# Kernel tuning notes

Measured on AMD Instinct MI355X. Metric: run time of the kernel, lower is better.

## Reference

```python
import jax, jax.numpy as jnp
import numpy as np

BETA = 0.25
EMA_DECAY = 0.99
EMA_EPS = 1e-05
K = 8192
D = 512


def setup_inputs() -> dict:
    key = jax.random.key(0)
    k1, k2, k3, k4 = jax.random.split(key, 4)
    z = jax.random.normal(k1, (8, 2048, D), dtype=jnp.float32)
    codebook_weight = jax.random.normal(k2, (K, D), dtype=jnp.float32)
    ema_cluster_size = jax.random.uniform(k3, (K,), dtype=jnp.float32)
    ema_embed_avg = jax.random.normal(k4, (K, D), dtype=jnp.float32)
    return {"z": z, "codebook_weight": codebook_weight,
            "ema_cluster_size": ema_cluster_size, "ema_embed_avg": ema_embed_avg}


def reference(z, codebook_weight, ema_cluster_size, ema_embed_avg):
    d = z.shape[-1]
    flat = z.reshape(-1, d)                                  # [N, D]
    z_sq = jnp.sum(flat * flat, axis=1, keepdims=True)       # [N, 1]
    e = codebook_weight                                      # [K, D]
    e_sq = jnp.sum(e * e, axis=1)                            # [K]
    # logits = -||z - e||^2 (argmax over logits == nearest code)
    logits = -(z_sq - 2.0 * jnp.matmul(flat, e.T) + e_sq)    # [N, K]
    idx = jnp.argmax(logits, axis=1)                         # [N]
    z_q = e[idx].reshape(z.shape)

    # commitment loss: beta * sum((z - sg[z_q])^2) / D
    vq_loss = BETA * jnp.sum((z - jax.lax.stop_gradient(z_q)) ** 2) / d

    # EMA statistics (torch.no_grad block)
    flat_sg = jax.lax.stop_gradient(flat)
    n_codes = e.shape[0]
    ones = jnp.ones(flat.shape[0], dtype=flat.dtype)
    cluster_size = jax.ops.segment_sum(ones, idx, num_segments=n_codes)       # == onehot.sum(0)
    embed_sum = jax.ops.segment_sum(flat_sg, idx, num_segments=n_codes)       # == onehot.T @ flat
    new_ema_cluster_size = ema_cluster_size * EMA_DECAY + cluster_size * (1.0 - EMA_DECAY)
    new_ema_embed_avg = ema_embed_avg * EMA_DECAY + embed_sum * (1.0 - EMA_DECAY)
    updated = new_ema_embed_avg / (new_ema_cluster_size[:, None] + EMA_EPS)
    active = (cluster_size > 0)[:, None]
    new_codebook = jnp.where(active, updated, codebook_weight)
    # (random reseeding of never-used codes is intentionally omitted: it is
    # nondeterministic and outside the deterministic math path)

    # straight-through estimator
    z_out = z + jax.lax.stop_gradient(z_q - z)
    return (z_out, vq_loss, new_ema_cluster_size, new_ema_embed_avg, new_codebook)
```

## Files before the change

### kernel.cpp

```cpp
#include <hip/hip_runtime.h>
#include <hip/hip_bf16.h>

#define N_ROWS 16384
#define DDIM   512
#define KCODES 8192
#define BETA   0.25f
#define DECAY  0.99f
#define ONE_MINUS_DECAY 0.01f
#define EMA_EPS 1e-5f

#define O_Z    0
#define O_LOSS 8388608
#define O_CS   8388609
#define O_AVG  8396801
#define O_CB   12591105

#define WS_CNT      0
#define WS_ESQ      32768
#define WS_FLAGCNT  65536
#define WS_FLAGLIST 65792
#define WS_KEYS     73984
#define WS_SEC2     205056
#define WS_LOSSP    270592
#define WS_IDXS     270848
#define WS_OFFS     336384
#define WS_CURS     369152
#define WS_ROWLIST  401920
#define WS_Z16      467456
#define WS_CB16     17244672

#define TAU  0.35f
#define RCAP 2048

typedef _Float16 half8  __attribute__((ext_vector_type(8)));
typedef float    floatx4 __attribute__((ext_vector_type(4)));

__device__ __forceinline__ unsigned enc_f(float d) {
    unsigned ub = __float_as_uint(d);
    return (ub & 0x80000000u) ? ~ub : (ub | 0x80000000u);
}
__device__ __forceinline__ float dec32(unsigned ub) {
    return __uint_as_float((ub & 0x80000000u) ? (ub ^ 0x80000000u) : ~ub);
}
__device__ __forceinline__ float dec_key(unsigned long long k) {
    return dec32((unsigned)(k >> 32));
}

__device__ __forceinline__ float4 pack8_f16(float4 a, float4 b) {
    auto p0 = __builtin_amdgcn_cvt_pkrtz(a.x, a.y);
    auto p1 = __builtin_amdgcn_cvt_pkrtz(a.z, a.w);
    auto p2 = __builtin_amdgcn_cvt_pkrtz(b.x, b.y);
    auto p3 = __builtin_amdgcn_cvt_pkrtz(b.z, b.w);
    float4 r;
    r.x = __builtin_bit_cast(float, p0);
    r.y = __builtin_bit_cast(float, p1);
    r.z = __builtin_bit_cast(float, p2);
    r.w = __builtin_bit_cast(float, p3);
    return r;
}

__device__ __forceinline__ void load_lds16(const void* g, void* l) {
    __builtin_amdgcn_global_load_lds(
        (const __attribute__((address_space(1))) unsigned int*)g,
        (__attribute__((address_space(3))) unsigned int*)l, 16, 0, 0);
}

__global__ __launch_bounds__(256) void cvtz_kernel(const float* __restrict__ z,
                                                   _Float16* __restrict__ z16,
                                                   unsigned long long* __restrict__ keys,
                                                   unsigned* __restrict__ sec2,
                                                   float* __restrict__ lossp,
                                                   int* __restrict__ flagcnt) {
    size_t i = (size_t)blockIdx.x * 256 + threadIdx.x;
    const float4* p = (const float4*)z + 2 * i;
    ((float4*)z16)[i] = pack8_f16(p[0], p[1]);
    if (i < N_ROWS) { keys[i] = ~0ULL; sec2[i] = 0xFFFFFFFFu; }
    if (i < 64) lossp[i] = 0.0f;
    if (i == 0) *flagcnt = 0;
}

__global__ __launch_bounds__(64) void cvtcb_kernel(const float* __restrict__ cb,
                                                   _Float16* __restrict__ cb16,
                                                   float* __restrict__ e_sq,
                                                   int* __restrict__ cnt) {
    int k = blockIdx.x;
    int t = threadIdx.x;
    const float4* r = (const float4*)(cb + (size_t)k * DDIM);
    float4 a = r[2 * t], b = r[2 * t + 1];
    ((float4*)(cb16 + (size_t)k * DDIM))[t] = pack8_f16(a, b);
    float s = a.x*a.x + a.y*a.y + a.z*a.z + a.w*a.w
            + b.x*b.x + b.y*b.y + b.z*b.z + b.w*b.w;
    #pragma unroll
    for (int o = 32; o > 0; o >>= 1) s += __shfl_down(s, o);
    if (t == 0) { e_sq[k] = s; cnt[k] = 0; }
}

__global__ __launch_bounds__(256, 4) void screen_kernel(
    const _Float16* __restrict__ z16, const _Float16* __restrict__ cb16,
    const float* __restrict__ e_sq,
    unsigned long long* __restrict__ keys, unsigned* __restrict__ sec2) {
    __shared__ _Float16 zt[128 * 64];
    __shared__ _Float16 ct[128 * 64];

    const int tid = threadIdx.x;
    const int by = blockIdx.x;
    const int bx = blockIdx.y;
    const int lane = tid & 63, wid = tid >> 6;
    const int wm = wid & 1, wn = wid >> 1;
    const int lr = lane & 15, lq = lane >> 4;

    const _Float16* zsrc[4]; const _Float16* csrc[4];
    #pragma unroll
    for (int r = 0; r < 4; r++) {
        int g = (r * 4 + wid) * 64 + lane;
        int row = g >> 3, kq = g & 7;
        zsrc[r] = z16 + (size_t)(by * 128 + row) * DDIM + ((kq ^ (row & 7)) << 3);
        csrc[r] = cb16 + (size_t)(bx * 128 + row) * DDIM + ((kq ^ (row & 7)) << 3);
    }

    floatx4 acc[4][4];
    #pragma unroll
    for (int i = 0; i < 4; i++)
        #pragma unroll
        for (int j = 0; j < 4; j++) acc[i][j] = floatx4{0.f, 0.f, 0.f, 0.f};

    for (int kc = 0; kc < DDIM; kc += 64) {
        #pragma unroll
        for (int r = 0; r < 4; r++) load_lds16(zsrc[r] + kc, &zt[(r * 4 + wid) * 512]);
        #pragma unroll
        for (int r = 0; r < 4; r++) load_lds16(csrc[r] + kc, &ct[(r * 4 + wid) * 512]);
        __syncthreads();
        #pragma unroll
        for (int kk = 0; kk < 2; kk++) {
            half8 av[4];
            #pragma unroll
            for (int mt = 0; mt < 4; mt++) {
                int row = wm * 64 + mt * 16 + lr;
                av[mt] = *(const half8*)&zt[row * 64 + (((kk * 4 + lq) ^ (row & 7)) << 3)];
            }
            #pragma unroll
            for (int nt = 0; nt < 4; nt++) {
                int row = wn * 64 + nt * 16 + lr;
                half8 bv = *(const half8*)&ct[row * 64 + (((kk * 4 + lq) ^ (row & 7)) << 3)];
                #pragma unroll
                for (int mt = 0; mt < 4; mt++)
                    acc[mt][nt] = __builtin_amdgcn_mfma_f32_16x16x32_f16(av[mt], bv, acc[mt][nt], 0, 0, 0);
            }
        }
        __syncthreads();
    }

    float* eb_d1 = (float*)zt;
    int*   eb_c1 = (int*)zt + 256;
    float* eb_d2 = (float*)zt + 512;

    float es[4];
    #pragma unroll
    for (int nt = 0; nt < 4; nt++) es[nt] = e_sq[bx * 128 + wn * 64 + nt * 16 + lr];

    #pragma unroll
    for (int mt = 0; mt < 4; mt++) {
        #pragma unroll
        for (int r = 0; r < 4; r++) {
            float d1 = 1e30f, d2 = 1e30f; int c1 = 0x7FFFFFFF;
            #pragma unroll
            for (int nt = 0; nt < 4; nt++) {
                float d = fmaf(-2.0f, acc[mt][nt][r], es[nt]);
                int c = bx * 128 + wn * 64 + nt * 16 + lr;
                bool better = (d < d1) || (d == d1 && c < c1);
                if (better) { d2 = d1; d1 = d; c1 = c; }
                else        { d2 = fminf(d2, d); }
            }
            #pragma unroll
            for (int off = 1; off < 16; off <<= 1) {
                float od1 = __shfl_xor(d1, off);
                int   oc1 = __shfl_xor(c1, off);
                float od2 = __shfl_xor(d2, off);
                bool better = (od1 < d1) || (od1 == d1 && oc1 < c1);
                if (better) { d2 = fminf(d1, od2); d1 = od1; c1 = oc1; }
                else        { d2 = fminf(d2, od1); }
            }
            if (lr == 0) {
                int row = wm * 64 + mt * 16 + lq * 4 + r;
                eb_d1[wn * 128 + row] = d1; eb_c1[wn * 128 + row] = c1; eb_d2[wn * 128 + row] = d2;
            }
        }
    }
    __syncthreads();
    if (tid < 128) {
        float d1a = eb_d1[tid],       d2a = eb_d2[tid];       int c1a = eb_c1[tid];
        float d1b = eb_d1[128 + tid], d2b = eb_d2[128 + tid]; int c1b = eb_c1[128 + tid];
        bool bbet = (d1b < d1a) || (d1b == d1a && c1b < c1a);
        float d1 = bbet ? d1b : d1a; int c1 = bbet ? c1b : c1a;
        float d2 = bbet ? fminf(d1a, d2b) : fminf(d2a, d1b);
        unsigned long long key = ((unsigned long long)enc_f(d1) << 32) | (unsigned)c1;
        int row_g = by * 128 + tid;
        unsigned long long old = atomicMin(&keys[row_g], key);
        float cand = (key < old) ? fminf(dec_key(old), d2) : fminf(d1, d2);
        atomicMin(&sec2[row_g], enc_f(cand));
    }
}

__global__ void merge_kernel(unsigned long long* __restrict__ keys,
                             const unsigned* __restrict__ sec2,
                             int* __restrict__ flagcnt, int* __restrict__ flaglist) {
    int row = blockIdx.x * 256 + threadIdx.x;
    unsigned long long kb = keys[row];
    float best = dec_key(kb);
    float sec  = dec32(sec2[row]);
    if (sec - best < TAU) {
        int pos = atomicAdd(flagcnt, 1);
        if (pos < RCAP) { flaglist[pos] = row; keys[row] = ~0ULL; }
    }
}

__global__ __launch_bounds__(256) void rescore_kernel(
    const float* __restrict__ z, const float* __restrict__ cb,
    const float* __restrict__ e_sq, const int* __restrict__ flagcnt,
    const int* __restrict__ flaglist, unsigned long long* __restrict__ keys) {
    int n = *flagcnt; n = min(n, RCAP);
    int base = blockIdx.y * 64;
    if (base >= n) return;
    __shared__ float ech[64][132];
    __shared__ float zch[64][68];
    __shared__ int ridx[64];
    const int tid = threadIdx.x;
    const int bx = blockIdx.x;
    if (tid < 64) ridx[tid] = flaglist[min(base + tid, n - 1)];
    __syncthreads();

    const int tc = tid & 15;
    const int tg = tid >> 4;

    float es[8];
    #pragma unroll
    for (int c = 0; c < 8; c++) es[c] = e_sq[bx * 128 + tc * 8 + c];

    float acc[4][8] = {};
    for (int kc = 0; kc < DDIM; kc += 64) {
        #pragma unroll
        for (int l = 0; l < 8; l++) {
            int gi = tid + 256 * l;
            int code = gi >> 4, q = gi & 15;
            float4 v = *(const float4*)&cb[(size_t)(bx * 128 + code) * DDIM + kc + q * 4];
            ech[q * 4 + 0][code] = v.x; ech[q * 4 + 1][code] = v.y;
            ech[q * 4 + 2][code] = v.z; ech[q * 4 + 3][code] = v.w;
        }
        #pragma unroll
        for (int l = 0; l < 4; l++) {
            int gi = tid + 256 * l;
            int row = gi >> 4, q = gi & 15;
            float4 v = *(const float4*)&z[(size_t)ridx[row] * DDIM + kc + q * 4];
            zch[q * 4 + 0][row] = v.x; zch[q * 4 + 1][row] = v.y;
            zch[q * 4 + 2][row] = v.z; zch[q * 4 + 3][row] = v.w;
        }
        __syncthreads();
        for (int k = 0; k < 64; k++) {
            const float4 b0 = *(const float4*)&ech[k][tc * 8];
            const float4 b1 = *(const float4*)&ech[k][tc * 8 + 4];
            const float4 a  = *(const float4*)&zch[k][tg * 4];
            const float ar[4] = {a.x, a.y, a.z, a.w};
            const float br[8] = {b0.x, b0.y, b0.z, b0.w, b1.x, b1.y, b1.z, b1.w};
            #pragma unroll
            for (int r = 0; r < 4; r++)
                #pragma unroll
                for (int c = 0; c < 8; c++)
                    acc[r][c] = fmaf(ar[r], br[c], acc[r][c]);
        }
        __syncthreads();
    }

    unsigned long long (*redk)[17] = (unsigned long long (*)[17])&ech[0][0];
    #pragma unroll
    for (int r = 0; r < 4; r++) {
        unsigned long long bk = ~0ULL;
        #pragma unroll
        for (int c = 0; c < 8; c++) {
            int code = bx * 128 + tc * 8 + c;
            float d = fmaf(-2.0f, acc[r][c], es[c]);
            unsigned long long key = ((unsigned long long)enc_f(d) << 32) | (unsigned)code;
            bk = (key < bk) ? key : bk;
        }
        redk[tg * 4 + r][tc] = bk;
    }
    __syncthreads();
    if (tid < 64) {
        unsigned long long b = redk[tid][0];
        #pragma unroll
        for (int t = 1; t < 16; t++) {
            unsigned long long v = redk[tid][t];
            b = (v < b) ? v : b;
        }
        atomicMin(&keys[ridx[tid]], b);
    }
}

__global__ __launch_bounds__(256) void zout_loss_kernel(
    const float* __restrict__ z, const float* __restrict__ cb,
    const unsigned long long* __restrict__ keys,
    float* __restrict__ out, int* __restrict__ cnt,
    int* __restrict__ idxs, float* __restrict__ lossp) {
    const int tid = threadIdx.x;
    const int sub = tid >> 7;
    const int t   = tid & 127;
    const int row = blockIdx.x * 2 + sub;
    const int idx = (int)(unsigned int)(keys[row] & 0xFFFFFFFFull);

    const float4 zv = ((const float4*)(z  + (size_t)row * DDIM))[t];
    const float4 ev = ((const float4*)(cb + (size_t)idx * DDIM))[t];
    ((float4*)(out + O_Z + (size_t)row * DDIM))[t] = ev;

    float dx = zv.x - ev.x, dy = zv.y - ev.y, dz = zv.z - ev.z, dw = zv.w - ev.w;
    float s = dx*dx + dy*dy + dz*dz + dw*dw;

    #pragma unroll
    for (int o = 32; o > 0; o >>= 1) s += __shfl_down(s, o);
    __shared__ float red[4];
    if ((tid & 63) == 0) red[tid >> 6] = s;
    __syncthreads();
    if (t == 0) {
        atomicAdd(&lossp[row & 63], red[sub * 2] + red[sub * 2 + 1]);
        atomicAdd(&cnt[idx], 1);
        idxs[row] = idx;
    }
}

__global__ __launch_bounds__(256) void scan_kernel(
    const int* __restrict__ cnt, const float* __restrict__ ema_cs,
    const float* __restrict__ lossp,
    float* __restrict__ out, int* __restrict__ offs, int* __restrict__ curs) {
    __shared__ int tot[256];
    const int t = threadIdx.x;
    if (t < 64) {
        float s = lossp[t];
        #pragma unroll
        for (int o = 32; o > 0; o >>= 1) s += __shfl_down(s, o);
        if (t == 0) out[O_LOSS] = s * (BETA / (float)DDIM);
    }
    const int base = t * 32;
    int local[32]; int s = 0;
    #pragma unroll
    for (int j = 0; j < 32; j++) { local[j] = cnt[base + j]; s += local[j]; }
    tot[t] = s;
    __syncthreads();
    for (int off = 1; off < 256; off <<= 1) {
        int v = (t >= off) ? tot[t - off] : 0;
        __syncthreads();
        tot[t] += v;
        __syncthreads();
    }
    int run = tot[t] - s;
    #pragma unroll
    for (int j = 0; j < 32; j++) {
        offs[base + j] = run; curs[base + j] = run;
        out[O_CS + base + j] = DECAY * ema_cs[base + j] + ONE_MINUS_DECAY * (float)local[j];
        run += local[j];
    }
}

__global__ void fill_kernel(const int* __restrict__ idxs, int* __restrict__ curs,
                            int* __restrict__ rowlist) {
    int row = blockIdx.x * 256 + threadIdx.x;
    int idx = idxs[row];
    int pos = atomicAdd(&curs[idx], 1);
    rowlist[pos] = row;
}

__global__ __launch_bounds__(256) void code_update_kernel(
    const float* __restrict__ z, const float* __restrict__ cb,
    const float* __restrict__ ema_cs, const float* __restrict__ ema_avg,
    const int* __restrict__ cnt, const int* __restrict__ offs,
    const int* __restrict__ rowlist, float* __restrict__ out) {
    const int lane = threadIdx.x & 63;
    const int k = blockIdx.x * 4 + (threadIdx.x >> 6);
    const int n = cnt[k], off = offs[k];
    float4 a0 = {0.f,0.f,0.f,0.f}, a1 = {0.f,0.f,0.f,0.f};
    for (int r = 0; r < n; r++) {
        int row = rowlist[off + r];
        const float4* zp = (const float4*)(z + (size_t)row * DDIM) + lane * 2;
        float4 v0 = zp[0], v1 = zp[1];
        a0.x += v0.x; a0.y += v0.y; a0.z += v0.z; a0.w += v0.w;
        a1.x += v1.x; a1.y += v1.y; a1.z += v1.z; a1.w += v1.w;
    }
    const float4* ep = (const float4*)(ema_avg + (size_t)k * DDIM) + lane * 2;
    float4 e0 = ep[0], e1 = ep[1];
    float4 n0, n1;
    n0.x = DECAY * e0.x + ONE_MINUS_DECAY * a0.x; n0.y = DECAY * e0.y + ONE_MINUS_DECAY * a0.y;
    n0.z = DECAY * e0.z + ONE_MINUS_DECAY * a0.z; n0.w = DECAY * e0.w + ONE_MINUS_DECAY * a0.w;
    n1.x = DECAY * e1.x + ONE_MINUS_DECAY * a1.x; n1.y = DECAY * e1.y + ONE_MINUS_DECAY * a1.y;
    n1.z = DECAY * e1.z + ONE_MINUS_DECAY * a1.z; n1.w = DECAY * e1.w + ONE_MINUS_DECAY * a1.w;
    ((float4*)(out + O_AVG + (size_t)k * DDIM))[lane * 2]     = n0;
    ((float4*)(out + O_AVG + (size_t)k * DDIM))[lane * 2 + 1] = n1;

    float ncs = DECAY * ema_cs[k] + ONE_MINUS_DECAY * (float)n;
    float inv = 1.0f / (ncs + EMA_EPS);
    float4 c0, c1;
    if (n > 0) {
        c0.x = n0.x * inv; c0.y = n0.y * inv; c0.z = n0.z * inv; c0.w = n0.w * inv;
        c1.x = n1.x * inv; c1.y = n1.y * inv; c1.z = n1.z * inv; c1.w = n1.w * inv;
    } else {
        const float4* cp = (const float4*)(cb + (size_t)k * DDIM) + lane * 2;
        c0 = cp[0]; c1 = cp[1];
    }
    ((float4*)(out + O_CB + (size_t)k * DDIM))[lane * 2]     = c0;
    ((float4*)(out + O_CB + (size_t)k * DDIM))[lane * 2 + 1] = c1;
}

extern "C" void kernel_launch(void* const* d_in, const int* in_sizes, int n_in,
                              void* d_out, int out_size, void* d_ws, size_t ws_size,
                              hipStream_t stream) {
    const float* z       = (const float*)d_in[0];
    const float* cb      = (const float*)d_in[1];
    const float* ema_cs  = (const float*)d_in[2];
    const float* ema_avg = (const float*)d_in[3];
    float* out = (float*)d_out;

    int* cnt       = (int*)((char*)d_ws + WS_CNT);
    float* e_sq    = (float*)((char*)d_ws + WS_ESQ);
    int* flagcnt   = (int*)((char*)d_ws + WS_FLAGCNT);
    int* flaglist  = (int*)((char*)d_ws + WS_FLAGLIST);
    unsigned long long* keys = (unsigned long long*)((char*)d_ws + WS_KEYS);
    unsigned* sec2 = (unsigned*)((char*)d_ws + WS_SEC2);
    float* lossp   = (float*)((char*)d_ws + WS_LOSSP);
    int* idxs      = (int*)((char*)d_ws + WS_IDXS);
    int* offs      = (int*)((char*)d_ws + WS_OFFS);
    int* curs      = (int*)((char*)d_ws + WS_CURS);
    int* rowlist   = (int*)((char*)d_ws + WS_ROWLIST);
    _Float16* z16  = (_Float16*)((char*)d_ws + WS_Z16);
    _Float16* cb16 = (_Float16*)((char*)d_ws + WS_CB16);

    cvtz_kernel<<<N_ROWS * DDIM / 8 / 256, 256, 0, stream>>>(z, z16, keys, sec2, lossp, flagcnt);
    cvtcb_kernel<<<KCODES, 64, 0, stream>>>(cb, cb16, e_sq, cnt);
    screen_kernel<<<dim3(N_ROWS / 128, KCODES / 128), 256, 0, stream>>>(z16, cb16, e_sq, keys, sec2);
    merge_kernel<<<N_ROWS / 256, 256, 0, stream>>>(keys, sec2, flagcnt, flaglist);
    rescore_kernel<<<dim3(KCODES / 128, RCAP / 64), 256, 0, stream>>>(z, cb, e_sq, flagcnt, flaglist, keys);
    zout_loss_kernel<<<N_ROWS / 2, 256, 0, stream>>>(z, cb, keys, out, cnt, idxs, lossp);
    scan_kernel<<<1, 256, 0, stream>>>(cnt, ema_cs, lossp, out, offs, curs);
    fill_kernel<<<N_ROWS / 256, 256, 0, stream>>>(idxs, curs, rowlist);
    code_update_kernel<<<KCODES / 4, 256, 0, stream>>>(z, cb, ema_cs, ema_avg, cnt, offs, rowlist, out);
}
```

Baseline: 627.9 us.

## Split screen kernel tile across 8 waves with 2x4 wave grid

The 128x128 distance-screen tile is now computed by 512 threads (8 waves arranged 2x4) instead of 256, so each wave holds 4x2 MFMA accumulators instead of 4x4. The global-to-LDS loads, the per-wave top-2 epilogue and the cross-wave merge (now over 4 column groups) are all adjusted to match. The aim is lower per-thread register use and more resident waves to hide memory and LDS latency. The cost is more LDS A-fragment reads per MFMA, since the z fragments are reloaded by four waves instead of two, plus a longer final merge.

```diff
diff --git a/kernel.cpp b/kernel.cpp
--- a/kernel.cpp
+++ b/kernel.cpp
@@ -95,7 +95,7 @@
     if (t == 0) { e_sq[k] = s; cnt[k] = 0; }
 }
 
-__global__ __launch_bounds__(256, 4) void screen_kernel(
+__global__ __launch_bounds__(512, 6) void screen_kernel(
     const _Float16* __restrict__ z16, const _Float16* __restrict__ cb16,
     const float* __restrict__ e_sq,
     unsigned long long* __restrict__ keys, unsigned* __restrict__ sec2) {
@@ -106,71 +106,68 @@
     const int by = blockIdx.x;
     const int bx = blockIdx.y;
     const int lane = tid & 63, wid = tid >> 6;
-    const int wm = wid & 1, wn = wid >> 1;
+    const int wm = wid >> 2, wn = wid & 3;
     const int lr = lane & 15, lq = lane >> 4;
 
-    const _Float16* zsrc[4]; const _Float16* csrc[4];
-    #pragma unroll
-    for (int r = 0; r < 4; r++) {
-        int g = (r * 4 + wid) * 64 + lane;
+    const _Float16* zsrc[2]; const _Float16* csrc[2];
+    #pragma unroll
+    for (int r = 0; r < 2; r++) {
+        int g = (r * 8 + wid) * 64 + lane;
         int row = g >> 3, kq = g & 7;
         zsrc[r] = z16 + (size_t)(by * 128 + row) * DDIM + ((kq ^ (row & 7)) << 3);
         csrc[r] = cb16 + (size_t)(bx * 128 + row) * DDIM + ((kq ^ (row & 7)) << 3);
     }
 
-    floatx4 acc[4][4];
+    floatx4 acc[4][2];
     #pragma unroll
     for (int i = 0; i < 4; i++)
         #pragma unroll
-        for (int j = 0; j < 4; j++) acc[i][j] = floatx4{0.f, 0.f, 0.f, 0.f};
+        for (int j = 0; j < 2; j++) acc[i][j] = floatx4{0.f, 0.f, 0.f, 0.f};
 
     for (int kc = 0; kc < DDIM; kc += 64) {
         #pragma unroll
-        for (int r = 0; r < 4; r++) load_lds16(zsrc[r] + kc, &zt[(r * 4 + wid) * 512]);
-        #pragma unroll
-        for (int r = 0; r < 4; r++) load_lds16(csrc[r] + kc, &ct[(r * 4 + wid) * 512]);
+        for (int r = 0; r < 2; r++) load_lds16(zsrc[r] + kc, &zt[(r * 8 + wid) * 512]);
+        #pragma unroll
+        for (int r = 0; r < 2; r++) load_lds16(csrc[r] + kc, &ct[(r * 8 + wid) * 512]);
         __syncthreads();
         #pragma unroll
         for (int kk = 0; kk < 2; kk++) {
-            half8 av[4];
+            half8 bv[2];
+            #pragma unroll
+            for (int nt = 0; nt < 2; nt++) {
+                int row = wn * 32 + nt * 16 + lr;
+                bv[nt] = *(const half8*)&ct[row * 64 + (((kk * 4 + lq) ^ (row & 7)) << 3)];
+            }
             #pragma unroll
             for (int mt = 0; mt < 4; mt++) {
                 int row = wm * 64 + mt * 16 + lr;
-                av[mt] = *(const half8*)&zt[row * 64 + (((kk * 4 + lq) ^ (row & 7)) << 3)];
+                half8 av = *(const half8*)&zt[row * 64 + (((kk * 4 + lq) ^ (row & 7)) << 3)];
+                acc[mt][0] = __builtin_amdgcn_mfma_f32_16x16x32_f16(av, bv[0], acc[mt][0], 0, 0, 0);
+                acc[mt][1] = __builtin_amdgcn_mfma_f32_16x16x32_f16(av, bv[1], acc[mt][1], 0, 0, 0);
             }
-            #pragma unroll
-            for (int nt = 0; nt < 4; nt++) {
-                int row = wn * 64 + nt * 16 + lr;
-                half8 bv = *(const half8*)&ct[row * 64 + (((kk * 4 + lq) ^ (row & 7)) << 3)];
-                #pragma unroll
-                for (int mt = 0; mt < 4; mt++)
-                    acc[mt][nt] = __builtin_amdgcn_mfma_f32_16x16x32_f16(av[mt], bv, acc[mt][nt], 0, 0, 0);
-            }
         }
         __syncthreads();
     }
 
     float* eb_d1 = (float*)zt;
-    int*   eb_c1 = (int*)zt + 256;
-    float* eb_d2 = (float*)zt + 512;
-
-    float es[4];
-    #pragma unroll
-    for (int nt = 0; nt < 4; nt++) es[nt] = e_sq[bx * 128 + wn * 64 + nt * 16 + lr];
+    int*   eb_c1 = (int*)zt + 512;
+    float* eb_d2 = (float*)zt + 1024;
+
+    float es[2];
+    #pragma unroll
+    for (int nt = 0; nt < 2; nt++) es[nt] = e_sq[bx * 128 + wn * 32 + nt * 16 + lr];
 
     #pragma unroll
     for (int mt = 0; mt < 4; mt++) {
         #pragma unroll
         for (int r = 0; r < 4; r++) {
-            float d1 = 1e30f, d2 = 1e30f; int c1 = 0x7FFFFFFF;
-            #pragma unroll
-            for (int nt = 0; nt < 4; nt++) {
-                float d = fmaf(-2.0f, acc[mt][nt][r], es[nt]);
-                int c = bx * 128 + wn * 64 + nt * 16 + lr;
-                bool better = (d < d1) || (d == d1 && c < c1);
-                if (better) { d2 = d1; d1 = d; c1 = c; }
-                else        { d2 = fminf(d2, d); }
-            }
+            float dA = fmaf(-2.0f, acc[mt][0][r], es[0]);
+            int   cA = bx * 128 + wn * 32 + lr;
+            float dB = fmaf(-2.0f, acc[mt][1][r], es[1]);
+            int   cB = bx * 128 + wn * 32 + 16 + lr;
+            bool bbet = (dB < dA) || (dB == dA && cB < cA);
+            float d1 = bbet ? dB : dA; int c1 = bbet ? cB : cA;
+            float d2 = bbet ? dA : dB;
             #pragma unroll
             for (int off = 1; off < 16; off <<= 1) {
                 float od1 = __shfl_xor(d1, off);
@@ -188,11 +185,14 @@
     }
     __syncthreads();
     if (tid < 128) {
-        float d1a = eb_d1[tid],       d2a = eb_d2[tid];       int c1a = eb_c1[tid];
-        float d1b = eb_d1[128 + tid], d2b = eb_d2[128 + tid]; int c1b = eb_c1[128 + tid];
-        bool bbet = (d1b < d1a) || (d1b == d1a && c1b < c1a);
-        float d1 = bbet ? d1b : d1a; int c1 = bbet ? c1b : c1a;
-        float d2 = bbet ? fminf(d1a, d2b) : fminf(d2a, d1b);
+        float d1 = eb_d1[tid], d2 = eb_d2[tid]; int c1 = eb_c1[tid];
+        #pragma unroll
+        for (int w = 1; w < 4; w++) {
+            float e1 = eb_d1[w * 128 + tid], e2 = eb_d2[w * 128 + tid]; int ec = eb_c1[w * 128 + tid];
+            bool bet = (e1 < d1) || (e1 == d1 && ec < c1);
+            if (bet) { d2 = fminf(d1, e2); d1 = e1; c1 = ec; }
+            else     { d2 = fminf(d2, e1); }
+        }
         unsigned long long key = ((unsigned long long)enc_f(d1) << 32) | (unsigned)c1;
         int row_g = by * 128 + tid;
         unsigned long long old = atomicMin(&keys[row_g], key);
@@ -431,7 +431,7 @@
 
     cvtz_kernel<<<N_ROWS * DDIM / 8 / 256, 256, 0, stream>>>(z, z16, keys, sec2, lossp, flagcnt);
     cvtcb_kernel<<<KCODES, 64, 0, stream>>>(cb, cb16, e_sq, cnt);
-    screen_kernel<<<dim3(N_ROWS / 128, KCODES / 128), 256, 0, stream>>>(z16, cb16, e_sq, keys, sec2);
+    screen_kernel<<<dim3(N_ROWS / 128, KCODES / 128), 512, 0, stream>>>(z16, cb16, e_sq, keys, sec2);
     merge_kernel<<<N_ROWS / 256, 256, 0, stream>>>(keys, sec2, flagcnt, flaglist);
     rescore_kernel<<<dim3(KCODES / 128, RCAP / 64), 256, 0, stream>>>(z, cb, e_sq, flagcnt, flaglist, keys);
     zout_loss_kernel<<<N_ROWS / 2, 256, 0, stream>>>(z, cb, keys, out, cnt, idxs, lossp);
```

Result: slower. 718.6 us (+14.4%).

## Replace sort-based EMA embed sum with float atomics and fuse prep kernels

Applied to the files above, without the earlier changes.

Merges the z and codebook conversion kernels into one prep kernel, which also writes the decayed ema_embed_avg into the output. The zout/loss kernel now atomically adds 0.01*z into the output average per assigned code. This replaces the scan, fill and gather-based code_update kernels with a single finalize kernel, cutting kernel launches and the serial single-block scan. The cost is 8M float atomics, possibly contended on popular codes, and a sum whose order varies between runs.

```diff
diff --git a/kernel.cpp b/kernel.cpp
--- a/kernel.cpp
+++ b/kernel.cpp
@@ -65,34 +65,43 @@
         (__attribute__((address_space(3))) unsigned int*)l, 16, 0, 0);
 }
 
-__global__ __launch_bounds__(256) void cvtz_kernel(const float* __restrict__ z,
-                                                   _Float16* __restrict__ z16,
-                                                   unsigned long long* __restrict__ keys,
-                                                   unsigned* __restrict__ sec2,
-                                                   float* __restrict__ lossp,
-                                                   int* __restrict__ flagcnt) {
-    size_t i = (size_t)blockIdx.x * 256 + threadIdx.x;
-    const float4* p = (const float4*)z + 2 * i;
-    ((float4*)z16)[i] = pack8_f16(p[0], p[1]);
-    if (i < N_ROWS) { keys[i] = ~0ULL; sec2[i] = 0xFFFFFFFFu; }
-    if (i < 64) lossp[i] = 0.0f;
-    if (i == 0) *flagcnt = 0;
-}
-
-__global__ __launch_bounds__(64) void cvtcb_kernel(const float* __restrict__ cb,
-                                                   _Float16* __restrict__ cb16,
-                                                   float* __restrict__ e_sq,
-                                                   int* __restrict__ cnt) {
-    int k = blockIdx.x;
-    int t = threadIdx.x;
-    const float4* r = (const float4*)(cb + (size_t)k * DDIM);
-    float4 a = r[2 * t], b = r[2 * t + 1];
-    ((float4*)(cb16 + (size_t)k * DDIM))[t] = pack8_f16(a, b);
-    float s = a.x*a.x + a.y*a.y + a.z*a.z + a.w*a.w
-            + b.x*b.x + b.y*b.y + b.z*b.z + b.w*b.w;
-    #pragma unroll
-    for (int o = 32; o > 0; o >>= 1) s += __shfl_down(s, o);
-    if (t == 0) { e_sq[k] = s; cnt[k] = 0; }
+__global__ __launch_bounds__(256) void prep_kernel(
+    const float* __restrict__ z, const float* __restrict__ cb,
+    const float* __restrict__ ema_avg,
+    _Float16* __restrict__ z16, _Float16* __restrict__ cb16,
+    float* __restrict__ e_sq, int* __restrict__ cnt,
+    unsigned long long* __restrict__ keys, unsigned* __restrict__ sec2,
+    float* __restrict__ lossp, int* __restrict__ flagcnt,
+    float* __restrict__ out) {
+    const int b = blockIdx.x, t = threadIdx.x;
+    if (b < 4096) {
+        size_t i = (size_t)b * 256 + t;
+        const float4* p = (const float4*)z + 2 * i;
+        ((float4*)z16)[i] = pack8_f16(p[0], p[1]);
+        if (i < N_ROWS) { keys[i] = ~0ULL; sec2[i] = 0xFFFFFFFFu; }
+        if (i < 64) lossp[i] = 0.0f;
+        if (i == 0) *flagcnt = 0;
+    } else if (b < 6144) {
+        const int k = (b - 4096) * 4 + (t >> 6);
+        const int tt = t & 63;
+        const float4* r = (const float4*)(cb + (size_t)k * DDIM);
+        float4 a = r[2 * tt], bb = r[2 * tt + 1];
+        ((float4*)(cb16 + (size_t)k * DDIM))[tt] = pack8_f16(a, bb);
+        float s = a.x*a.x + a.y*a.y + a.z*a.z + a.w*a.w
+                + bb.x*bb.x + bb.y*bb.y + bb.z*bb.z + bb.w*bb.w;
+        #pragma unroll
+        for (int o = 32; o > 0; o >>= 1) s += __shfl_down(s, o);
+        if (tt == 0) { e_sq[k] = s; cnt[k] = 0; }
+    } else {
+        size_t i = (size_t)(b - 6144) * 256 + t;
+        const float4* ep = (const float4*)ema_avg + 2 * i;
+        float4 e0 = ep[0], e1 = ep[1];
+        float4 o0, o1;
+        o0.x = DECAY * e0.x; o0.y = DECAY * e0.y; o0.z = DECAY * e0.z; o0.w = DECAY * e0.w;
+        o1.x = DECAY * e1.x; o1.y = DECAY * e1.y; o1.z = DECAY * e1.z; o1.w = DECAY * e1.w;
+        ((float4*)(out + O_AVG))[2 * i]     = o0;
+        ((float4*)(out + O_AVG))[2 * i + 1] = o1;
+    }
 }
 
 __global__ __launch_bounds__(256, 4) void screen_kernel(
@@ -299,7 +308,7 @@
     const float* __restrict__ z, const float* __restrict__ cb,
     const unsigned long long* __restrict__ keys,
     float* __restrict__ out, int* __restrict__ cnt,
-    int* __restrict__ idxs, float* __restrict__ lossp) {
+    float* __restrict__ lossp) {
     const int tid = threadIdx.x;
     const int sub = tid >> 7;
     const int t   = tid & 127;
@@ -312,6 +321,12 @@
 
     float dx = zv.x - ev.x, dy = zv.y - ev.y, dz = zv.z - ev.z, dw = zv.w - ev.w;
     float s = dx*dx + dy*dy + dz*dz + dw*dw;
+
+    float* ap = out + O_AVG + (size_t)idx * DDIM + t * 4;
+    atomicAdd(ap + 0, ONE_MINUS_DECAY * zv.x);
+    atomicAdd(ap + 1, ONE_MINUS_DECAY * zv.y);
+    atomicAdd(ap + 2, ONE_MINUS_DECAY * zv.z);
+    atomicAdd(ap + 3, ONE_MINUS_DECAY * zv.w);
 
     #pragma unroll
     for (int o = 32; o > 0; o >>= 1) s += __shfl_down(s, o);
@@ -321,83 +336,33 @@
     if (t == 0) {
         atomicAdd(&lossp[row & 63], red[sub * 2] + red[sub * 2 + 1]);
         atomicAdd(&cnt[idx], 1);
-        idxs[row] = idx;
-    }
-}
-
-__global__ __launch_bounds__(256) void scan_kernel(
-    const int* __restrict__ cnt, const float* __restrict__ ema_cs,
-    const float* __restrict__ lossp,
-    float* __restrict__ out, int* __restrict__ offs, int* __restrict__ curs) {
-    __shared__ int tot[256];
-    const int t = threadIdx.x;
-    if (t < 64) {
-        float s = lossp[t];
+    }
+}
+
+__global__ __launch_bounds__(256) void finalize_kernel(
+    const float* __restrict__ cb, const float* __restrict__ ema_cs,
+    const int* __restrict__ cnt, const float* __restrict__ lossp,
+    float* __restrict__ out) {
+    const int tid = threadIdx.x;
+    if (blockIdx.x == 0 && tid < 64) {
+        float s = lossp[tid];
         #pragma unroll
         for (int o = 32; o > 0; o >>= 1) s += __shfl_down(s, o);
-        if (t == 0) out[O_LOSS] = s * (BETA / (float)DDIM);
-    }
-    const int base = t * 32;
-    int local[32]; int s = 0;
-    #pragma unroll
-    for (int j = 0; j < 32; j++) { local[j] = cnt[base + j]; s += local[j]; }
-    tot[t] = s;
-    __syncthreads();
-    for (int off = 1; off < 256; off <<= 1) {
-        int v = (t >= off) ? tot[t - off] : 0;
-        __syncthreads();
-        tot[t] += v;
-        __syncthreads();
-    }
-    int run = tot[t] - s;
-    #pragma unroll
-    for (int j = 0; j < 32; j++) {
-        offs[base + j] = run; curs[base + j] = run;
-        out[O_CS + base + j] = DECAY * ema_cs[base + j] + ONE_MINUS_DECAY * (float)local[j];
-        run += local[j];
-    }
-}
-
-__global__ void fill_kernel(const int* __restrict__ idxs, int* __restrict__ curs,
-                            int* __restrict__ rowlist) {
-    int row = blockIdx.x * 256 + threadIdx.x;
-    int idx = idxs[row];
-    int pos = atomicAdd(&curs[idx], 1);
-    rowlist[pos] = row;
-}
-
-__global__ __launch_bounds__(256) void code_update_kernel(
-    const float* __restrict__ z, const float* __restrict__ cb,
-    const float* __restrict__ ema_cs, const float* __restrict__ ema_avg,
-    const int* __restrict__ cnt, const int* __restrict__ offs,
-    const int* __restrict__ rowlist, float* __restrict__ out) {
-    const int lane = threadIdx.x & 63;
-    const int k = blockIdx.x * 4 + (threadIdx.x >> 6);
-    const int n = cnt[k], off = offs[k];
-    float4 a0 = {0.f,0.f,0.f,0.f}, a1 = {0.f,0.f,0.f,0.f};
-    for (int r = 0; r < n; r++) {
-        int row = rowlist[off + r];
-        const float4* zp = (const float4*)(z + (size_t)row * DDIM) + lane * 2;
-        float4 v0 = zp[0], v1 = zp[1];
-        a0.x += v0.x; a0.y += v0.y; a0.z += v0.z; a0.w += v0.w;
-        a1.x += v1.x; a1.y += v1.y; a1.z += v1.z; a1.w += v1.w;
-    }
-    const float4* ep = (const float4*)(ema_avg + (size_t)k * DDIM) + lane * 2;
-    float4 e0 = ep[0], e1 = ep[1];
-    float4 n0, n1;
-    n0.x = DECAY * e0.x + ONE_MINUS_DECAY * a0.x; n0.y = DECAY * e0.y + ONE_MINUS_DECAY * a0.y;
-    n0.z = DECAY * e0.z + ONE_MINUS_DECAY * a0.z; n0.w = DECAY * e0.w + ONE_MINUS_DECAY * a0.w;
-    n1.x = DECAY * e1.x + ONE_MINUS_DECAY * a1.x; n1.y = DECAY * e1.y + ONE_MINUS_DECAY * a1.y;
-    n1.z = DECAY * e1.z + ONE_MINUS_DECAY * a1.z; n1.w = DECAY * e1.w + ONE_MINUS_DECAY * a1.w;
-    ((float4*)(out + O_AVG + (size_t)k * DDIM))[lane * 2]     = n0;
-    ((float4*)(out + O_AVG + (size_t)k * DDIM))[lane * 2 + 1] = n1;
-
+        if (tid == 0) out[O_LOSS] = s * (BETA / (float)DDIM);
+    }
+    const int lane = tid & 63;
+    const int k = blockIdx.x * 4 + (tid >> 6);
+    const int n = cnt[k];
     float ncs = DECAY * ema_cs[k] + ONE_MINUS_DECAY * (float)n;
-    float inv = 1.0f / (ncs + EMA_EPS);
+    if (lane == 0) out[O_CS + k] = ncs;
+
     float4 c0, c1;
     if (n > 0) {
-        c0.x = n0.x * inv; c0.y = n0.y * inv; c0.z = n0.z * inv; c0.w = n0.w * inv;
-        c1.x = n1.x * inv; c1.y = n1.y * inv; c1.z = n1.z * inv; c1.w = n1.w * inv;
+        const float inv = 1.0f / (ncs + EMA_EPS);
+        const float4* ap = (const float4*)(out + O_AVG + (size_t)k * DDIM) + lane * 2;
+        float4 a0 = ap[0], a1 = ap[1];
+        c0.x = a0.x * inv; c0.y = a0.y * inv; c0.z = a0.z * inv; c0.w = a0.w * inv;
+        c1.x = a1.x * inv; c1.y = a1.y * inv; c1.z = a1.z * inv; c1.w = a1.w * inv;
     } else {
         const float4* cp = (const float4*)(cb + (size_t)k * DDIM) + lane * 2;
         c0 = cp[0]; c1 = cp[1];
@@ -422,20 +387,14 @@
     unsigned long long* keys = (unsigned long long*)((char*)d_ws + WS_KEYS);
     unsigned* sec2 = (unsigned*)((char*)d_ws + WS_SEC2);
     float* lossp   = (float*)((char*)d_ws + WS_LOSSP);
-    int* idxs      = (int*)((char*)d_ws + WS_IDXS);
-    int* offs      = (int*)((char*)d_ws + WS_OFFS);
-    int* curs      = (int*)((char*)d_ws + WS_CURS);
-    int* rowlist   = (int*)((char*)d_ws + WS_ROWLIST);
     _Float16* z16  = (_Float16*)((char*)d_ws + WS_Z16);
     _Float16* cb16 = (_Float16*)((char*)d_ws + WS_CB16);
 
-    cvtz_kernel<<<N_ROWS * DDIM / 8 / 256, 256, 0, stream>>>(z, z16, keys, sec2, lossp, flagcnt);
-    cvtcb_kernel<<<KCODES, 64, 0, stream>>>(cb, cb16, e_sq, cnt);
+    prep_kernel<<<8192, 256, 0, stream>>>(z, cb, ema_avg, z16, cb16, e_sq, cnt,
+                                          keys, sec2, lossp, flagcnt, out);
     screen_kernel<<<dim3(N_ROWS / 128, KCODES / 128), 256, 0, stream>>>(z16, cb16, e_sq, keys, sec2);
     merge_kernel<<<N_ROWS / 256, 256, 0, stream>>>(keys, sec2, flagcnt, flaglist);
     rescore_kernel<<<dim3(KCODES / 128, RCAP / 64), 256, 0, stream>>>(z, cb, e_sq, flagcnt, flaglist, keys);
-    zout_loss_kernel<<<N_ROWS / 2, 256, 0, stream>>>(z, cb, keys, out, cnt, idxs, lossp);
-    scan_kernel<<<1, 256, 0, stream>>>(cnt, ema_cs, lossp, out, offs, curs);
-    fill_kernel<<<N_ROWS / 256, 256, 0, stream>>>(idxs, curs, rowlist);
-    code_update_kernel<<<KCODES / 4, 256, 0, stream>>>(z, cb, ema_cs, ema_avg, cnt, offs, rowlist, out);
-}
+    zout_loss_kernel<<<N_ROWS / 2, 256, 0, stream>>>(z, cb, keys, out, cnt, lossp);
+    finalize_kernel<<<KCODES / 4, 256, 0, stream>>>(cb, ema_cs, cnt, lossp, out);
+}
```

New measurement: 618.8 us. Within noise of the previous version (-1.4%).
